# Kernel tuning notes

Hardware: AMD Instinct MI355X
Metric: run time of the kernel (lower is better)

## Reference

```python
import jax, jax.numpy as jnp
import numpy as np
import math

STRIDE = 32
CTR_CLAMP = 32.0
SCALE_CLAMP = math.log(1000.0 / 16)  # DEFAULT_SCALE_CLAMP
CONF_THRESH = 0.05
NMS_THRESH = 0.6
TOPK = 1000
NUM_CLASSES = 80
CLASS_OFFSET = 1.0e5  # separates classes so one IoU pass == per-class NMS


def setup_inputs() -> dict:
    key = jax.random.key(0)
    k1, k2 = jax.random.split(key)
    fmp_h, fmp_w = 100, 100
    A = 5
    M = fmp_h * fmp_w * A  # 50000 candidates
    cls_pred = jax.random.normal(k1, (M, NUM_CLASSES), dtype=jnp.float32)
    reg_pred = jax.random.normal(k2, (M, 4), dtype=jnp.float32)
    anchor_size = jnp.array([[32, 32], [64, 64], [128, 128], [256, 256], [512, 512]], dtype=jnp.float32)
    return {"cls_pred": cls_pred, "reg_pred": reg_pred, "anchor_size": anchor_size,
            "fmp_h": fmp_h, "fmp_w": fmp_w}


def _generate_anchors(anchor_size, fmp_h, fmp_w):
    # anchors laid out as [H*W, A, 4] -> [M, 4], matching torch.meshgrid order
    ys, xs = jnp.meshgrid(jnp.arange(fmp_h, dtype=jnp.float32),
                          jnp.arange(fmp_w, dtype=jnp.float32), indexing="ij")
    xy = (jnp.stack([xs, ys], axis=-1).reshape(-1, 2) + 0.5) * STRIDE  # [HW, 2]
    A = anchor_size.shape[0]
    anchor_xy = jnp.repeat(xy[:, None, :], A, axis=1)                   # [HW, A, 2]
    anchor_wh = jnp.broadcast_to(anchor_size[None], (xy.shape[0], A, 2))
    return jnp.concatenate([anchor_xy, anchor_wh], axis=-1).reshape(-1, 4)  # [M, 4]


def _decode_boxes(anchors, reg):
    # anchors/reg: [K, 4] (cx, cy, w, h) / (dx, dy, dw, dh)
    ctr_off = jnp.clip(reg[:, :2] * anchors[:, 2:], -CTR_CLAMP, CTR_CLAMP)
    ctr_xy = anchors[:, :2] + ctr_off
    wh = anchors[:, 2:] * jnp.exp(jnp.minimum(reg[:, 2:], SCALE_CLAMP))
    return jnp.concatenate([ctr_xy - 0.5 * wh, ctr_xy + 0.5 * wh], axis=-1)  # x1y1x2y2


def _greedy_nms_keep(boxes, valid):
    # boxes: [K, 4] already score-sorted descending; valid: [K] bool
    x1, y1, x2, y2 = boxes[:, 0], boxes[:, 1], boxes[:, 2], boxes[:, 3]
    areas = (x2 - x1) * (y2 - y1)
    xx1 = jnp.maximum(x1[:, None], x1[None, :])
    yy1 = jnp.maximum(y1[:, None], y1[None, :])
    xx2 = jnp.minimum(x2[:, None], x2[None, :])
    yy2 = jnp.minimum(y2[:, None], y2[None, :])
    inter = jnp.maximum(1e-28, xx2 - xx1) * jnp.maximum(1e-28, yy2 - yy1)
    iou = inter / (areas[:, None] + areas[None, :] - inter + 1e-14)  # [K, K]
    idxs = jnp.arange(boxes.shape[0])

    def body(i, keep):
        suppress = keep[i] & (iou[i] > NMS_THRESH) & (idxs > i)
        return keep & ~suppress

    return jax.lax.fori_loop(0, boxes.shape[0], body, valid)


def reference(cls_pred, reg_pred, anchor_size, fmp_h, fmp_w):
    anchors = _generate_anchors(anchor_size, fmp_h, fmp_w)  # [M, 4]
    probs = jax.nn.sigmoid(cls_pred)                        # [M, C]
    scores = probs.max(axis=-1)
    labels = probs.argmax(axis=-1)
    # top-k candidates (lax.top_k returns scores sorted descending)
    scores, idx = jax.lax.top_k(scores, TOPK)
    labels = labels[idx]
    reg = reg_pred[idx]
    anc = anchors[idx]
    boxes = _decode_boxes(anc, reg)                         # [K, 4] in pixels
    valid = scores >= CONF_THRESH
    # per-class NMS via class offsets (boxes of different classes never overlap)
    boxes_off = boxes + labels.astype(boxes.dtype)[:, None] * CLASS_OFFSET
    keep = _greedy_nms_keep(boxes_off, valid)
    img_w = fmp_w * STRIDE
    img_h = fmp_h * STRIDE
    scale = jnp.array([img_w, img_h, img_w, img_h], dtype=boxes.dtype)
    nboxes = jnp.clip(boxes / scale, 0.0, 1.0)
    m = keep.astype(boxes.dtype)
    return nboxes * m[:, None], scores * m, jnp.where(keep, labels, -1), keep
```

## Files before the change

kernel.cpp:

```cpp
#include <hip/hip_runtime.h>
#include <math.h>

#define NCLS 80
#define TOPK 1000
#define CAND_CAP 4096

__device__ __forceinline__ float sigmoid_np(float x) {
  float e = (float)exp(-(double)x);
  return 1.0f / (1.0f + e);
}
__device__ __forceinline__ float exp_np(float x) { return (float)exp((double)x); }

__device__ __forceinline__ unsigned fkey(float s) {
  unsigned u = __float_as_uint(s);
  return ((int)u < 0) ? ~u : (u | 0x80000000u);
}

#define KEY_BASE 0xBF000000u
__device__ __forceinline__ unsigned kbin(unsigned key) { return (key >> 11) & 0xFFFu; }

__device__ __forceinline__ void agg_add(unsigned* h, unsigned bin, bool pred) {
  unsigned long long rem = __ballot(pred);
  const int lane = threadIdx.x & 63;
  while (rem) {
    int leader = __ffsll(rem) - 1;
    unsigned lb = (unsigned)__shfl((int)bin, leader, 64);
    unsigned long long m = __ballot(pred && bin == lb);
    if (lane == leader) atomicAdd(&h[lb], (unsigned)__popcll(m));
    rem &= ~m;
  }
}

__global__ void k_zero(unsigned* __restrict__ p, int nwords) {
  int i = blockIdx.x * 256 + threadIdx.x;
  if (i < nwords) p[i] = 0u;
}

__launch_bounds__(1024)
__global__ void k_score(const float* __restrict__ cls, float* __restrict__ scores,
                        int* __restrict__ labels, unsigned* __restrict__ ghist1, int M) {
  __shared__ unsigned h1[4096];
  const int t = threadIdx.x;
  #pragma unroll
  for (int k = 0; k < 4; ++k) h1[t + 1024 * k] = 0u;
  __syncthreads();

  int gid = blockIdx.x * 1024 + t;
  int anchor = gid >> 2;
  int q = gid & 3;
  bool act = anchor < M;
  float lv[20];
  float best = -3.4e38f; int bc = 0;
  if (act) {
    const float4* row = reinterpret_cast<const float4*>(cls) + (size_t)anchor * (NCLS / 4);
    #pragma unroll
    for (int k = 0; k < 5; ++k) {
      float4 v = row[q + 4 * k];
      int cbase = (q + 4 * k) * 4;
      lv[4 * k + 0] = v.x; lv[4 * k + 1] = v.y; lv[4 * k + 2] = v.z; lv[4 * k + 3] = v.w;
      if (v.x > best) { best = v.x; bc = cbase + 0; }
      if (v.y > best) { best = v.y; bc = cbase + 1; }
      if (v.z > best) { best = v.z; bc = cbase + 2; }
      if (v.w > best) { best = v.w; bc = cbase + 3; }
    }
  } else {
    #pragma unroll
    for (int k = 0; k < 20; ++k) lv[k] = -3.4e38f;
  }
  #pragma unroll
  for (int d = 1; d < 4; d <<= 1) {
    float ob = __shfl_xor(best, d, 64);
    int oc = __shfl_xor(bc, d, 64);
    if (ob > best || (ob == best && oc < bc)) { best = ob; bc = oc; }
  }
  float s = sigmoid_np(best);
  float sp = s * (1.0f - s);
  float band = (s < 1.0f && sp > 0.0f) ? (4.8e-7f / sp) : 3.4e38f;
  float thresh = best - band;
  int cclose = 1 << 30;
  #pragma unroll
  for (int k = 0; k < 5; ++k) {
    #pragma unroll
    for (int j = 0; j < 4; ++j) {
      int c = (q + 4 * k) * 4 + j;
      if (lv[4 * k + j] >= thresh && c < cclose) cclose = c;
    }
  }
  #pragma unroll
  for (int d = 1; d < 4; d <<= 1) {
    int oc = __shfl_xor(cclose, d, 64);
    if (oc < cclose) cclose = oc;
  }
  int lab = bc;
  if (act && cclose < bc && q == 0) {
    float bp = -1.0f; int bl = 0;
    for (int c = 0; c < NCLS; ++c) {
      float p = sigmoid_np(cls[(size_t)anchor * NCLS + c]);
      if (p > bp) { bp = p; bl = c; }
    }
    lab = bl;
  }
  unsigned key = fkey(s);
  if (act && q == 0) {
    scores[anchor] = s;
    labels[anchor] = lab;
  }
  agg_add(h1, kbin(key), act && q == 0 && key >= KEY_BASE);
  __syncthreads();
  #pragma unroll
  for (int k = 0; k < 4; ++k) {
    unsigned c = h1[t + 1024 * k];
    if (c) atomicAdd(&ghist1[t + 1024 * k], c);
  }
}

__launch_bounds__(1024)
__global__ void k_compact(const unsigned* __restrict__ ghist1, const float* __restrict__ scores,
                          unsigned long long* __restrict__ cand, unsigned* __restrict__ gcount,
                          int M) {
  __shared__ unsigned chunks[1024];
  __shared__ int sB1;
  __shared__ unsigned wcnt[16];
  __shared__ unsigned sbase;
  const int t = threadIdx.x;
  const int lane = t & 63, wid = t >> 6;
  if (t == 0) sB1 = 0;

  unsigned hb0 = ghist1[4 * t], hb1 = ghist1[4 * t + 1],
           hb2 = ghist1[4 * t + 2], hb3 = ghist1[4 * t + 3];
  chunks[t] = hb0 + hb1 + hb2 + hb3;
  __syncthreads();
  for (int d = 1; d < 1024; d <<= 1) {
    unsigned v = chunks[t] + ((t + d < 1024) ? chunks[t + d] : 0u);
    __syncthreads(); chunks[t] = v; __syncthreads();
  }
  {
    unsigned ssc = chunks[t];
    unsigned ssn = (t + 1 < 1024) ? chunks[t + 1] : 0u;
    if (ssc >= (unsigned)TOPK && ssn < (unsigned)TOPK) {
      unsigned hb[4] = {hb0, hb1, hb2, hb3};
      unsigned run = ssn;
      for (int b = 3; b >= 0; --b) {
        run += hb[b];
        if (run >= (unsigned)TOPK) { sB1 = 4 * t + b; break; }
      }
    }
  }
  __syncthreads();
  const unsigned T = KEY_BASE + ((unsigned)sB1 << 11);

  int base = (blockIdx.x * 1024 + t) * 4;
  unsigned keys[4]; int idxs[4]; int np = 0;
  if (base + 3 < M) {
    float4 v = *reinterpret_cast<const float4*>(scores + base);
    unsigned kk[4] = {fkey(v.x), fkey(v.y), fkey(v.z), fkey(v.w)};
    #pragma unroll
    for (int j = 0; j < 4; ++j)
      if (kk[j] >= T) { keys[np] = kk[j]; idxs[np] = base + j; ++np; }
  } else {
    for (int i = base; i < M; ++i) {
      unsigned key = fkey(scores[i]);
      if (key >= T) { keys[np] = key; idxs[np] = i; ++np; }
    }
  }
  int sc = np;
  #pragma unroll
  for (int d = 1; d < 64; d <<= 1) {
    int o = __shfl_up(sc, d, 64);
    if (lane >= d) sc += o;
  }
  if (lane == 63) wcnt[wid] = (unsigned)sc;
  __syncthreads();
  if (t == 0) {
    unsigned acc = 0;
    for (int w = 0; w < 16; ++w) { unsigned v = wcnt[w]; wcnt[w] = acc; acc += v; }
    sbase = acc ? atomicAdd(gcount, acc) : 0u;
  }
  __syncthreads();
  unsigned pos = sbase + wcnt[wid] + (unsigned)(sc - np);
  for (int j = 0; j < np; ++j) {
    if (pos < (unsigned)CAND_CAP)
      cand[pos] = ((unsigned long long)keys[j] << 32) | (unsigned)(~(unsigned)idxs[j]);
    ++pos;
  }
}

__launch_bounds__(1024)
__global__ void k_rank(const unsigned long long* __restrict__ cand, const unsigned* __restrict__ gcount,
                       const int* __restrict__ labels, const float* __restrict__ reg,
                       const float* __restrict__ asz, const int* __restrict__ pW, int A,
                       float* __restrict__ sel_score, int* __restrict__ sel_label,
                       float* __restrict__ boxes, float* __restrict__ areas,
                       float* __restrict__ obox) {
  __shared__ unsigned long long ck[CAND_CAP];
  const int t = threadIdx.x;
  unsigned n = *gcount; if (n > (unsigned)CAND_CAP) n = (unsigned)CAND_CAP;
  for (int i = t; i < (int)n; i += 1024) ck[i] = cand[i];
  __syncthreads();
  for (int cc = 0; cc < CAND_CAP; cc += 1024) {
    if ((unsigned)cc >= n) break;
    int c = cc + t;
    bool actv = (unsigned)c < n;
    unsigned long long my = actv ? ck[c] : 0ull;
    int r = 0;
    for (int j = 0; j < (int)n; ++j) r += (ck[j] > my);
    if (actv && r < TOPK) {
      unsigned key = (unsigned)(my >> 32);
      unsigned u = (key & 0x80000000u) ? (key ^ 0x80000000u) : ~key;
      float scv = __uint_as_float(u);
      int idx = (int)(~(unsigned)my);
      int lab = labels[idx];
      int W = *pW;
      int a = idx % A;
      int cell = idx / A;
      int x = cell % W;
      int y = cell / W;
      float aw = asz[a * 2 + 0], ah = asz[a * 2 + 1];
      float ax = ((float)x + 0.5f) * 32.0f;
      float ay = ((float)y + 0.5f) * 32.0f;
      float4 rg = *reinterpret_cast<const float4*>(reg + (size_t)idx * 4);
      float offx = fminf(fmaxf(rg.x * aw, -32.0f), 32.0f);
      float offy = fminf(fmaxf(rg.y * ah, -32.0f), 32.0f);
      float cx = ax + offx, cy = ay + offy;
      const float SC = 4.135166556742356f;
      float bw = aw * exp_np(fminf(rg.z, SC));
      float bh = ah * exp_np(fminf(rg.w, SC));
      float x1 = cx - 0.5f * bw, y1 = cy - 0.5f * bh;
      float x2 = cx + 0.5f * bw, y2 = cy + 0.5f * bh;
      float off = (float)lab * 100000.0f;
      float ox1 = x1 + off, oy1 = y1 + off, ox2 = x2 + off, oy2 = y2 + off;
      sel_score[r] = scv; sel_label[r] = lab;
      boxes[r * 4 + 0] = x1; boxes[r * 4 + 1] = y1;
      boxes[r * 4 + 2] = x2; boxes[r * 4 + 3] = y2;
      obox[0 * 1024 + r] = ox1; obox[1 * 1024 + r] = oy1;
      obox[2 * 1024 + r] = ox2; obox[3 * 1024 + r] = oy2;
      areas[r] = (ox2 - ox1) * (oy2 - oy1);
    }
  }
}

__launch_bounds__(1024)
__global__ void k_mask(const float* __restrict__ obox, const float* __restrict__ areas,
                       unsigned long long* __restrict__ maskC) {
  __shared__ float so0[1024], so1[1024], so2[1024], so3[1024], sa[1024];
  const int t = threadIdx.x;
  const int c = blockIdx.x, j = t;
  so0[t] = obox[t];        so1[t] = obox[1024 + t];
  so2[t] = obox[2048 + t]; so3[t] = obox[3072 + t];
  sa[t] = areas[t];
  __syncthreads();
  unsigned long long bits = 0ull;
  if (j < TOPK) {
    float x1j = so0[j], y1j = so1[j], x2j = so2[j], y2j = so3[j];
    float aj = sa[j];
    int i0 = c * 64;
    for (int ii = 0; ii < 64; ++ii) {
      int i = i0 + ii;
      if (i < TOPK && i < j) {
        float xx1 = fmaxf(so0[i], x1j);
        float yy1 = fmaxf(so1[i], y1j);
        float xx2 = fminf(so2[i], x2j);
        float yy2 = fminf(so3[i], y2j);
        float inter = fmaxf(1e-28f, xx2 - xx1) * fmaxf(1e-28f, yy2 - yy1);
        float uni = sa[i] + aj - inter + 1e-14f;
        float iou = inter / uni;
        if (iou > 0.6f) bits |= (1ull << ii);
      }
    }
  }
  maskC[c * 1024 + j] = bits;
}

__launch_bounds__(512)
__global__ void k_nms(const unsigned long long* __restrict__ maskC,
                      const float* __restrict__ sel_score, const int* __restrict__ sel_label,
                      const float* __restrict__ boxes,
                      const int* __restrict__ pW, const int* __restrict__ pH,
                      float* __restrict__ out) {
  __shared__ unsigned long long sm[16 * 1024];
  __shared__ float ssc[1024];
  __shared__ unsigned long long kwS[16];
  const int tid = threadIdx.x;
  const int lane = tid & 63;

  {
    const float4* g4 = reinterpret_cast<const float4*>(maskC);
    float4* s4 = reinterpret_cast<float4*>(sm);
    float4 v[16];
    #pragma unroll
    for (int k = 0; k < 16; ++k) v[k] = g4[tid + k * 512];
    #pragma unroll
    for (int k = 0; k < 16; ++k) s4[tid + k * 512] = v[k];
  }
  #pragma unroll
  for (int k = 0; k < 2; ++k) {
    int i = tid + k * 512;
    ssc[i] = (i < TOPK) ? sel_score[i] : 0.0f;
  }
  __syncthreads();

  if (tid < 64) {
    unsigned long long supp[16];
    #pragma unroll
    for (int f = 0; f < 16; ++f) supp[f] = 0ull;
    #pragma unroll
    for (int f = 0; f < 16; ++f) {
      unsigned long long ct = sm[f * 1024 + f * 64 + lane];
      int r = f * 64 + lane;
      unsigned long long valid = __ballot((r < TOPK) && (ssc[r] >= 0.05f));
      unsigned long long sup_any = __ballot(ct != 0ull);
      unsigned long long avail = valid & ~supp[f];
      unsigned long long kwf = 0ull;
      while (avail) {
        unsigned long long fs = avail & sup_any;
        if (!fs) { kwf |= avail; break; }
        int i = __ffsll((long long)fs) - 1;
        unsigned long long below = (1ull << i) - 1ull;
        kwf |= avail & below;
        kwf |= (1ull << i);
        unsigned long long vict = __ballot(((ct >> i) & 1ull) != 0ull);
        avail &= ~vict;
        avail &= ~(below | (1ull << i));
      }
      if (lane == 0) kwS[f] = kwf;
      #pragma unroll
      for (int g = f + 1; g < 16; ++g)
        supp[g] |= __ballot((sm[f * 1024 + g * 64 + lane] & kwf) != 0ull);
    }
  }
  __syncthreads();

  float sw = (float)(*pW * 32);
  float sh = (float)(*pH * 32);
  const float4* b4 = reinterpret_cast<const float4*>(boxes);
  for (int r = tid; r < TOPK; r += 512) {
    bool kp = (kwS[r >> 6] >> (r & 63)) & 1ull;
    float m = kp ? 1.0f : 0.0f;
    float4 b = b4[r];
    float b0 = fminf(fmaxf(b.x / sw, 0.0f), 1.0f) * m;
    float b1 = fminf(fmaxf(b.y / sh, 0.0f), 1.0f) * m;
    float b2 = fminf(fmaxf(b.z / sw, 0.0f), 1.0f) * m;
    float b3 = fminf(fmaxf(b.w / sh, 0.0f), 1.0f) * m;
    out[r * 4 + 0] = b0; out[r * 4 + 1] = b1;
    out[r * 4 + 2] = b2; out[r * 4 + 3] = b3;
    out[TOPK * 4 + r] = ssc[r] * m;
    out[TOPK * 5 + r] = kp ? (float)sel_label[r] : -1.0f;
    out[TOPK * 6 + r] = m;
  }
}

extern "C" void kernel_launch(void* const* d_in, const int* in_sizes, int n_in,
                              void* d_out, int out_size, void* d_ws, size_t ws_size,
                              hipStream_t stream) {
  const float* cls = (const float*)d_in[0];
  const float* reg = (const float*)d_in[1];
  const float* asz = (const float*)d_in[2];
  const int* pH = (const int*)d_in[3];
  const int* pW = (const int*)d_in[4];
  int M = in_sizes[0] / NCLS;
  int A = in_sizes[2] / 2;

  char* ws = (char*)d_ws;
  size_t off = 0;
  auto alloc = [&](size_t bytes) { size_t o = off; off = (off + bytes + 255) & ~(size_t)255; return o; };
  size_t o_h1   = alloc(4096 * sizeof(unsigned));
  size_t o_cnt  = alloc(256);
  size_t zero_end = off;
  size_t o_cand = alloc((size_t)CAND_CAP * sizeof(unsigned long long));
  size_t o_sc   = alloc((size_t)M * sizeof(float));
  size_t o_lb   = alloc((size_t)M * sizeof(int));
  size_t o_ssc  = alloc(1024 * sizeof(float));
  size_t o_slb  = alloc(1024 * sizeof(int));
  size_t o_box  = alloc((size_t)TOPK * 4 * sizeof(float));
  size_t o_area = alloc(1024 * sizeof(float));
  size_t o_obox = alloc(4 * 1024 * sizeof(float));
  size_t o_mask = alloc((size_t)16 * 1024 * sizeof(unsigned long long));
  (void)ws_size; (void)out_size; (void)n_in;

  int zwords = (int)(zero_end / 4);
  k_zero<<<(zwords + 255) / 256, 256, 0, stream>>>((unsigned*)ws, zwords);
  int nblk_score = (M * 4 + 1023) / 1024;
  k_score<<<nblk_score, 1024, 0, stream>>>(
      cls, (float*)(ws + o_sc), (int*)(ws + o_lb), (unsigned*)(ws + o_h1), M);
  int nblk_cmp = ((M + 3) / 4 + 1023) / 1024;
  k_compact<<<nblk_cmp, 1024, 0, stream>>>(
      (const unsigned*)(ws + o_h1), (const float*)(ws + o_sc),
      (unsigned long long*)(ws + o_cand), (unsigned*)(ws + o_cnt), M);
  k_rank<<<1, 1024, 0, stream>>>(
      (const unsigned long long*)(ws + o_cand), (const unsigned*)(ws + o_cnt),
      (const int*)(ws + o_lb), reg, asz, pW, A,
      (float*)(ws + o_ssc), (int*)(ws + o_slb),
      (float*)(ws + o_box), (float*)(ws + o_area), (float*)(ws + o_obox));
  k_mask<<<16, 1024, 0, stream>>>(
      (const float*)(ws + o_obox), (const float*)(ws + o_area),
      (unsigned long long*)(ws + o_mask));
  k_nms<<<1, 512, 0, stream>>>(
      (const unsigned long long*)(ws + o_mask),
      (const float*)(ws + o_ssc), (const int*)(ws + o_slb),
      (const float*)(ws + o_box), pW, pH, (float*)d_out);
}
```

Before: 74.49 us.

## Fuse compact+rank and mask+NMS kernels via last-block-done pattern

Merges the candidate compaction with the ranking/decode stage, and the IoU mask stage with the greedy NMS stage. Each pair becomes one launch where the last block to finish, detected via an atomic counter and threadfence, performs the serial tail. The NMS part now loads only the upper-triangular mask tiles into a union-shared LDS buffer. This removes two kernel launches and their dependency gaps, but makes one block do the tail work while others exit, and relies on extra zeroed counters.

```diff
diff --git a/kernel.cpp b/kernel.cpp
--- a/kernel.cpp
+++ b/kernel.cpp
@@ -4,6 +4,7 @@
 #define NCLS 80
 #define TOPK 1000
 #define CAND_CAP 4096
+#define TRI_IDX(f, g) ((f) * 16 - ((f) * ((f) - 1)) / 2 + ((g) - (f)))
 
 __device__ __forceinline__ float sigmoid_np(float x) {
   float e = (float)exp(-(double)x);
@@ -115,13 +116,21 @@
 }
 
 __launch_bounds__(1024)
-__global__ void k_compact(const unsigned* __restrict__ ghist1, const float* __restrict__ scores,
-                          unsigned long long* __restrict__ cand, unsigned* __restrict__ gcount,
-                          int M) {
+__global__ void k_cr(const unsigned* __restrict__ ghist1, const float* __restrict__ scores,
+                     unsigned long long* __restrict__ cand, unsigned* __restrict__ gcount,
+                     unsigned* __restrict__ done,
+                     const int* __restrict__ labels, const float* __restrict__ reg,
+                     const float* __restrict__ asz, const int* __restrict__ pW,
+                     int M, int A,
+                     float* __restrict__ sel_score, int* __restrict__ sel_label,
+                     float* __restrict__ boxes, float* __restrict__ areas,
+                     float* __restrict__ obox) {
   __shared__ unsigned chunks[1024];
+  __shared__ unsigned long long ck[CAND_CAP];
   __shared__ int sB1;
   __shared__ unsigned wcnt[16];
   __shared__ unsigned sbase;
+  __shared__ bool sLast;
   const int t = threadIdx.x;
   const int lane = t & 63, wid = t >> 6;
   if (t == 0) sB1 = 0;
@@ -183,17 +192,14 @@
       cand[pos] = ((unsigned long long)keys[j] << 32) | (unsigned)(~(unsigned)idxs[j]);
     ++pos;
   }
-}
-
-__launch_bounds__(1024)
-__global__ void k_rank(const unsigned long long* __restrict__ cand, const unsigned* __restrict__ gcount,
-                       const int* __restrict__ labels, const float* __restrict__ reg,
-                       const float* __restrict__ asz, const int* __restrict__ pW, int A,
-                       float* __restrict__ sel_score, int* __restrict__ sel_label,
-                       float* __restrict__ boxes, float* __restrict__ areas,
-                       float* __restrict__ obox) {
-  __shared__ unsigned long long ck[CAND_CAP];
-  const int t = threadIdx.x;
+
+  __threadfence();
+  __syncthreads();
+  if (t == 0) sLast = (atomicAdd(done, 1u) == (unsigned)(gridDim.x - 1));
+  __syncthreads();
+  if (!sLast) return;
+  __threadfence();
+
   unsigned n = *gcount; if (n > (unsigned)CAND_CAP) n = (unsigned)CAND_CAP;
   for (int i = t; i < (int)n; i += 1024) ck[i] = cand[i];
   __syncthreads();
@@ -239,75 +245,82 @@
   }
 }
 
+union MnLds {
+  struct { float so0[1024], so1[1024], so2[1024], so3[1024], sa[1024]; } m;
+  struct { unsigned long long sm[8704]; float ssc[1024];
+           int pf[136], pg[136]; unsigned long long kwS[16]; } n;
+};
+
 __launch_bounds__(1024)
-__global__ void k_mask(const float* __restrict__ obox, const float* __restrict__ areas,
-                       unsigned long long* __restrict__ maskC) {
-  __shared__ float so0[1024], so1[1024], so2[1024], so3[1024], sa[1024];
+__global__ void k_mn(const float* __restrict__ obox, const float* __restrict__ areas,
+                     unsigned long long* __restrict__ maskC, unsigned* __restrict__ done,
+                     const float* __restrict__ sel_score, const int* __restrict__ sel_label,
+                     const float* __restrict__ boxes,
+                     const int* __restrict__ pW, const int* __restrict__ pH,
+                     float* __restrict__ out) {
+  __shared__ MnLds L;
+  __shared__ bool sLast;
   const int t = threadIdx.x;
+  const int lane = t & 63;
   const int c = blockIdx.x, j = t;
-  so0[t] = obox[t];        so1[t] = obox[1024 + t];
-  so2[t] = obox[2048 + t]; so3[t] = obox[3072 + t];
-  sa[t] = areas[t];
-  __syncthreads();
-  unsigned long long bits = 0ull;
-  if (j < TOPK) {
-    float x1j = so0[j], y1j = so1[j], x2j = so2[j], y2j = so3[j];
-    float aj = sa[j];
-    int i0 = c * 64;
-    for (int ii = 0; ii < 64; ++ii) {
-      int i = i0 + ii;
-      if (i < TOPK && i < j) {
-        float xx1 = fmaxf(so0[i], x1j);
-        float yy1 = fmaxf(so1[i], y1j);
-        float xx2 = fminf(so2[i], x2j);
-        float yy2 = fminf(so3[i], y2j);
-        float inter = fmaxf(1e-28f, xx2 - xx1) * fmaxf(1e-28f, yy2 - yy1);
-        float uni = sa[i] + aj - inter + 1e-14f;
-        float iou = inter / uni;
-        if (iou > 0.6f) bits |= (1ull << ii);
+
+  L.m.so0[t] = obox[t];        L.m.so1[t] = obox[1024 + t];
+  L.m.so2[t] = obox[2048 + t]; L.m.so3[t] = obox[3072 + t];
+  L.m.sa[t] = areas[t];
+  __syncthreads();
+  {
+    unsigned long long bits = 0ull;
+    if (j < TOPK) {
+      float x1j = L.m.so0[j], y1j = L.m.so1[j], x2j = L.m.so2[j], y2j = L.m.so3[j];
+      float aj = L.m.sa[j];
+      int i0 = c * 64;
+      for (int ii = 0; ii < 64; ++ii) {
+        int i = i0 + ii;
+        if (i < TOPK && i < j) {
+          float xx1 = fmaxf(L.m.so0[i], x1j);
+          float yy1 = fmaxf(L.m.so1[i], y1j);
+          float xx2 = fminf(L.m.so2[i], x2j);
+          float yy2 = fminf(L.m.so3[i], y2j);
+          float inter = fmaxf(1e-28f, xx2 - xx1) * fmaxf(1e-28f, yy2 - yy1);
+          float uni = L.m.sa[i] + aj - inter + 1e-14f;
+          float iou = inter / uni;
+          if (iou > 0.6f) bits |= (1ull << ii);
+        }
       }
     }
-  }
-  maskC[c * 1024 + j] = bits;
-}
-
-__launch_bounds__(512)
-__global__ void k_nms(const unsigned long long* __restrict__ maskC,
-                      const float* __restrict__ sel_score, const int* __restrict__ sel_label,
-                      const float* __restrict__ boxes,
-                      const int* __restrict__ pW, const int* __restrict__ pH,
-                      float* __restrict__ out) {
-  __shared__ unsigned long long sm[16 * 1024];
-  __shared__ float ssc[1024];
-  __shared__ unsigned long long kwS[16];
-  const int tid = threadIdx.x;
-  const int lane = tid & 63;
-
-  {
-    const float4* g4 = reinterpret_cast<const float4*>(maskC);
-    float4* s4 = reinterpret_cast<float4*>(sm);
-    float4 v[16];
-    #pragma unroll
-    for (int k = 0; k < 16; ++k) v[k] = g4[tid + k * 512];
-    #pragma unroll
-    for (int k = 0; k < 16; ++k) s4[tid + k * 512] = v[k];
-  }
-  #pragma unroll
-  for (int k = 0; k < 2; ++k) {
-    int i = tid + k * 512;
-    ssc[i] = (i < TOPK) ? sel_score[i] : 0.0f;
-  }
-  __syncthreads();
-
-  if (tid < 64) {
+    maskC[c * 1024 + j] = bits;
+  }
+
+  __threadfence();
+  __syncthreads();
+  if (t == 0) sLast = (atomicAdd(done, 1u) == (unsigned)(gridDim.x - 1));
+  __syncthreads();
+  if (!sLast) return;
+  __threadfence();
+  __syncthreads();
+
+  if (t < 136) {
+    int p = t, f = 0;
+    while (p >= 16 - f) { p -= 16 - f; ++f; }
+    L.n.pf[t] = f; L.n.pg[t] = f + p;
+  }
+  L.n.ssc[t] = (t < TOPK) ? sel_score[t] : 0.0f;
+  __syncthreads();
+  for (int i = t; i < 136 * 64; i += 1024) {
+    int p = i >> 6, l = i & 63;
+    L.n.sm[i] = maskC[L.n.pf[p] * 1024 + L.n.pg[p] * 64 + l];
+  }
+  __syncthreads();
+
+  if (t < 64) {
     unsigned long long supp[16];
     #pragma unroll
     for (int f = 0; f < 16; ++f) supp[f] = 0ull;
     #pragma unroll
     for (int f = 0; f < 16; ++f) {
-      unsigned long long ct = sm[f * 1024 + f * 64 + lane];
+      unsigned long long ct = L.n.sm[TRI_IDX(f, f) * 64 + lane];
       int r = f * 64 + lane;
-      unsigned long long valid = __ballot((r < TOPK) && (ssc[r] >= 0.05f));
+      unsigned long long valid = __ballot((r < TOPK) && (L.n.ssc[r] >= 0.05f));
       unsigned long long sup_any = __ballot(ct != 0ull);
       unsigned long long avail = valid & ~supp[f];
       unsigned long long kwf = 0ull;
@@ -322,10 +335,10 @@
         avail &= ~vict;
         avail &= ~(below | (1ull << i));
       }
-      if (lane == 0) kwS[f] = kwf;
+      if (lane == 0) L.n.kwS[f] = kwf;
       #pragma unroll
       for (int g = f + 1; g < 16; ++g)
-        supp[g] |= __ballot((sm[f * 1024 + g * 64 + lane] & kwf) != 0ull);
+        supp[g] |= __ballot((L.n.sm[TRI_IDX(f, g) * 64 + lane] & kwf) != 0ull);
     }
   }
   __syncthreads();
@@ -333,8 +346,9 @@
   float sw = (float)(*pW * 32);
   float sh = (float)(*pH * 32);
   const float4* b4 = reinterpret_cast<const float4*>(boxes);
-  for (int r = tid; r < TOPK; r += 512) {
-    bool kp = (kwS[r >> 6] >> (r & 63)) & 1ull;
+  if (t < TOPK) {
+    int r = t;
+    bool kp = (L.n.kwS[r >> 6] >> (r & 63)) & 1ull;
     float m = kp ? 1.0f : 0.0f;
     float4 b = b4[r];
     float b0 = fminf(fmaxf(b.x / sw, 0.0f), 1.0f) * m;
@@ -343,7 +357,7 @@
     float b3 = fminf(fmaxf(b.w / sh, 0.0f), 1.0f) * m;
     out[r * 4 + 0] = b0; out[r * 4 + 1] = b1;
     out[r * 4 + 2] = b2; out[r * 4 + 3] = b3;
-    out[TOPK * 4 + r] = ssc[r] * m;
+    out[TOPK * 4 + r] = L.n.ssc[r] * m;
     out[TOPK * 5 + r] = kp ? (float)sel_label[r] : -1.0f;
     out[TOPK * 6 + r] = m;
   }
@@ -383,19 +397,16 @@
   k_score<<<nblk_score, 1024, 0, stream>>>(
       cls, (float*)(ws + o_sc), (int*)(ws + o_lb), (unsigned*)(ws + o_h1), M);
   int nblk_cmp = ((M + 3) / 4 + 1023) / 1024;
-  k_compact<<<nblk_cmp, 1024, 0, stream>>>(
+  k_cr<<<nblk_cmp, 1024, 0, stream>>>(
       (const unsigned*)(ws + o_h1), (const float*)(ws + o_sc),
-      (unsigned long long*)(ws + o_cand), (unsigned*)(ws + o_cnt), M);
-  k_rank<<<1, 1024, 0, stream>>>(
-      (const unsigned long long*)(ws + o_cand), (const unsigned*)(ws + o_cnt),
-      (const int*)(ws + o_lb), reg, asz, pW, A,
+      (unsigned long long*)(ws + o_cand), (unsigned*)(ws + o_cnt),
+      (unsigned*)(ws + o_cnt + 4),
+      (const int*)(ws + o_lb), reg, asz, pW, M, A,
       (float*)(ws + o_ssc), (int*)(ws + o_slb),
       (float*)(ws + o_box), (float*)(ws + o_area), (float*)(ws + o_obox));
-  k_mask<<<16, 1024, 0, stream>>>(
+  k_mn<<<16, 1024, 0, stream>>>(
       (const float*)(ws + o_obox), (const float*)(ws + o_area),
-      (unsigned long long*)(ws + o_mask));
-  k_nms<<<1, 512, 0, stream>>>(
-      (const unsigned long long*)(ws + o_mask),
+      (unsigned long long*)(ws + o_mask), (unsigned*)(ws + o_cnt + 8),
       (const float*)(ws + o_ssc), (const int*)(ws + o_slb),
       (const float*)(ws + o_box), pW, pH, (float*)d_out);
 }
```

New measurement: 86.55 us. 16.2% more time.

## Fuse top-k ranking into IoU mask kernel and load only upper-triangle mask tiles

Applied to the files above, without the earlier changes.

The single-block rank kernel is merged into the 16-block mask kernel. Each block now redundantly ranks all candidates and decodes boxes into shared memory, then computes its own 64-column IoU slice, which removes one launch and the global round trip for the decoded boxes and areas. The NMS kernel grows to 1024 threads and loads only the 136 upper-triangular 64x64 mask tiles into a packed shared array instead of all 256. The cost is that the O(n^2) rank work is repeated in all 16 blocks, and the fused kernel's larger shared-memory footprint may limit occupancy.

```diff
diff --git a/kernel.cpp b/kernel.cpp
--- a/kernel.cpp
+++ b/kernel.cpp
@@ -4,6 +4,7 @@
 #define NCLS 80
 #define TOPK 1000
 #define CAND_CAP 4096
+#define TRI_IDX(f, g) ((f) * 16 - ((f) * ((f) - 1)) / 2 + ((g) - (f)))
 
 __device__ __forceinline__ float sigmoid_np(float x) {
   float e = (float)exp(-(double)x);
@@ -186,22 +187,31 @@
 }
 
 __launch_bounds__(1024)
-__global__ void k_rank(const unsigned long long* __restrict__ cand, const unsigned* __restrict__ gcount,
-                       const int* __restrict__ labels, const float* __restrict__ reg,
-                       const float* __restrict__ asz, const int* __restrict__ pW, int A,
-                       float* __restrict__ sel_score, int* __restrict__ sel_label,
-                       float* __restrict__ boxes, float* __restrict__ areas,
-                       float* __restrict__ obox) {
+__global__ void k_maskr(const unsigned long long* __restrict__ cand,
+                        const unsigned* __restrict__ gcount,
+                        const int* __restrict__ labels, const float* __restrict__ reg,
+                        const float* __restrict__ asz, const int* __restrict__ pW, int A,
+                        float* __restrict__ sel_score, int* __restrict__ sel_label,
+                        float* __restrict__ boxes,
+                        unsigned long long* __restrict__ maskC) {
   __shared__ unsigned long long ck[CAND_CAP];
+  __shared__ float so0[1024], so1[1024], so2[1024], so3[1024], sa[1024];
+  __shared__ float4 bx[1024];
+  __shared__ float ssc[1024]; __shared__ int slab[1024];
   const int t = threadIdx.x;
+  const int c = blockIdx.x;
+
+  ssc[t] = 0.0f; slab[t] = 0;
+  so0[t] = 0.0f; so1[t] = 0.0f; so2[t] = 0.0f; so3[t] = 0.0f; sa[t] = 0.0f;
   unsigned n = *gcount; if (n > (unsigned)CAND_CAP) n = (unsigned)CAND_CAP;
   for (int i = t; i < (int)n; i += 1024) ck[i] = cand[i];
   __syncthreads();
+
   for (int cc = 0; cc < CAND_CAP; cc += 1024) {
     if ((unsigned)cc >= n) break;
-    int c = cc + t;
-    bool actv = (unsigned)c < n;
-    unsigned long long my = actv ? ck[c] : 0ull;
+    int cidx = cc + t;
+    bool actv = (unsigned)cidx < n;
+    unsigned long long my = actv ? ck[cidx] : 0ull;
     int r = 0;
     for (int j = 0; j < (int)n; ++j) r += (ck[j] > my);
     if (actv && r < TOPK) {
@@ -229,83 +239,78 @@
       float x2 = cx + 0.5f * bw, y2 = cy + 0.5f * bh;
       float off = (float)lab * 100000.0f;
       float ox1 = x1 + off, oy1 = y1 + off, ox2 = x2 + off, oy2 = y2 + off;
-      sel_score[r] = scv; sel_label[r] = lab;
-      boxes[r * 4 + 0] = x1; boxes[r * 4 + 1] = y1;
-      boxes[r * 4 + 2] = x2; boxes[r * 4 + 3] = y2;
-      obox[0 * 1024 + r] = ox1; obox[1 * 1024 + r] = oy1;
-      obox[2 * 1024 + r] = ox2; obox[3 * 1024 + r] = oy2;
-      areas[r] = (ox2 - ox1) * (oy2 - oy1);
-    }
+      ssc[r] = scv; slab[r] = lab;
+      bx[r] = make_float4(x1, y1, x2, y2);
+      so0[r] = ox1; so1[r] = oy1; so2[r] = ox2; so3[r] = oy2;
+      sa[r] = (ox2 - ox1) * (oy2 - oy1);
+    }
+  }
+  __syncthreads();
+
+  if (c == 0) {
+    sel_score[t] = ssc[t];
+    sel_label[t] = slab[t];
+    reinterpret_cast<float4*>(boxes)[t] = bx[t];
+  }
+
+  {
+    int j = t;
+    unsigned long long bits = 0ull;
+    if (j < TOPK) {
+      float x1j = so0[j], y1j = so1[j], x2j = so2[j], y2j = so3[j];
+      float aj = sa[j];
+      int i0 = c * 64;
+      for (int ii = 0; ii < 64; ++ii) {
+        int i = i0 + ii;
+        if (i < TOPK && i < j) {
+          float xx1 = fmaxf(so0[i], x1j);
+          float yy1 = fmaxf(so1[i], y1j);
+          float xx2 = fminf(so2[i], x2j);
+          float yy2 = fminf(so3[i], y2j);
+          float inter = fmaxf(1e-28f, xx2 - xx1) * fmaxf(1e-28f, yy2 - yy1);
+          float uni = sa[i] + aj - inter + 1e-14f;
+          float iou = inter / uni;
+          if (iou > 0.6f) bits |= (1ull << ii);
+        }
+      }
+    }
+    maskC[c * 1024 + j] = bits;
   }
 }
 
 __launch_bounds__(1024)
-__global__ void k_mask(const float* __restrict__ obox, const float* __restrict__ areas,
-                       unsigned long long* __restrict__ maskC) {
-  __shared__ float so0[1024], so1[1024], so2[1024], so3[1024], sa[1024];
-  const int t = threadIdx.x;
-  const int c = blockIdx.x, j = t;
-  so0[t] = obox[t];        so1[t] = obox[1024 + t];
-  so2[t] = obox[2048 + t]; so3[t] = obox[3072 + t];
-  sa[t] = areas[t];
-  __syncthreads();
-  unsigned long long bits = 0ull;
-  if (j < TOPK) {
-    float x1j = so0[j], y1j = so1[j], x2j = so2[j], y2j = so3[j];
-    float aj = sa[j];
-    int i0 = c * 64;
-    for (int ii = 0; ii < 64; ++ii) {
-      int i = i0 + ii;
-      if (i < TOPK && i < j) {
-        float xx1 = fmaxf(so0[i], x1j);
-        float yy1 = fmaxf(so1[i], y1j);
-        float xx2 = fminf(so2[i], x2j);
-        float yy2 = fminf(so3[i], y2j);
-        float inter = fmaxf(1e-28f, xx2 - xx1) * fmaxf(1e-28f, yy2 - yy1);
-        float uni = sa[i] + aj - inter + 1e-14f;
-        float iou = inter / uni;
-        if (iou > 0.6f) bits |= (1ull << ii);
-      }
-    }
-  }
-  maskC[c * 1024 + j] = bits;
-}
-
-__launch_bounds__(512)
 __global__ void k_nms(const unsigned long long* __restrict__ maskC,
                       const float* __restrict__ sel_score, const int* __restrict__ sel_label,
                       const float* __restrict__ boxes,
                       const int* __restrict__ pW, const int* __restrict__ pH,
                       float* __restrict__ out) {
-  __shared__ unsigned long long sm[16 * 1024];
+  __shared__ unsigned long long sm[136 * 64];
   __shared__ float ssc[1024];
   __shared__ unsigned long long kwS[16];
-  const int tid = threadIdx.x;
-  const int lane = tid & 63;
-
-  {
-    const float4* g4 = reinterpret_cast<const float4*>(maskC);
-    float4* s4 = reinterpret_cast<float4*>(sm);
-    float4 v[16];
-    #pragma unroll
-    for (int k = 0; k < 16; ++k) v[k] = g4[tid + k * 512];
-    #pragma unroll
-    for (int k = 0; k < 16; ++k) s4[tid + k * 512] = v[k];
-  }
-  #pragma unroll
-  for (int k = 0; k < 2; ++k) {
-    int i = tid + k * 512;
-    ssc[i] = (i < TOPK) ? sel_score[i] : 0.0f;
-  }
-  __syncthreads();
-
-  if (tid < 64) {
+  __shared__ int pf[136], pg[136];
+  const int t = threadIdx.x;
+  const int lane = t & 63;
+
+  if (t < 136) {
+    int p = t, f = 0;
+    while (p >= 16 - f) { p -= 16 - f; ++f; }
+    pf[t] = f; pg[t] = f + p;
+  }
+  ssc[t] = (t < TOPK) ? sel_score[t] : 0.0f;
+  __syncthreads();
+  for (int i = t; i < 136 * 64; i += 1024) {
+    int p = i >> 6, l = i & 63;
+    sm[i] = maskC[pf[p] * 1024 + pg[p] * 64 + l];
+  }
+  __syncthreads();
+
+  if (t < 64) {
     unsigned long long supp[16];
     #pragma unroll
     for (int f = 0; f < 16; ++f) supp[f] = 0ull;
     #pragma unroll
     for (int f = 0; f < 16; ++f) {
-      unsigned long long ct = sm[f * 1024 + f * 64 + lane];
+      unsigned long long ct = sm[TRI_IDX(f, f) * 64 + lane];
       int r = f * 64 + lane;
       unsigned long long valid = __ballot((r < TOPK) && (ssc[r] >= 0.05f));
       unsigned long long sup_any = __ballot(ct != 0ull);
@@ -325,7 +330,7 @@
       if (lane == 0) kwS[f] = kwf;
       #pragma unroll
       for (int g = f + 1; g < 16; ++g)
-        supp[g] |= __ballot((sm[f * 1024 + g * 64 + lane] & kwf) != 0ull);
+        supp[g] |= __ballot((sm[TRI_IDX(f, g) * 64 + lane] & kwf) != 0ull);
     }
   }
   __syncthreads();
@@ -333,7 +338,8 @@
   float sw = (float)(*pW * 32);
   float sh = (float)(*pH * 32);
   const float4* b4 = reinterpret_cast<const float4*>(boxes);
-  for (int r = tid; r < TOPK; r += 512) {
+  if (t < TOPK) {
+    int r = t;
     bool kp = (kwS[r >> 6] >> (r & 63)) & 1ull;
     float m = kp ? 1.0f : 0.0f;
     float4 b = b4[r];
@@ -371,9 +377,7 @@
   size_t o_lb   = alloc((size_t)M * sizeof(int));
   size_t o_ssc  = alloc(1024 * sizeof(float));
   size_t o_slb  = alloc(1024 * sizeof(int));
-  size_t o_box  = alloc((size_t)TOPK * 4 * sizeof(float));
-  size_t o_area = alloc(1024 * sizeof(float));
-  size_t o_obox = alloc(4 * 1024 * sizeof(float));
+  size_t o_box  = alloc(1024 * 4 * sizeof(float));
   size_t o_mask = alloc((size_t)16 * 1024 * sizeof(unsigned long long));
   (void)ws_size; (void)out_size; (void)n_in;
 
@@ -386,15 +390,12 @@
   k_compact<<<nblk_cmp, 1024, 0, stream>>>(
       (const unsigned*)(ws + o_h1), (const float*)(ws + o_sc),
       (unsigned long long*)(ws + o_cand), (unsigned*)(ws + o_cnt), M);
-  k_rank<<<1, 1024, 0, stream>>>(
+  k_maskr<<<16, 1024, 0, stream>>>(
       (const unsigned long long*)(ws + o_cand), (const unsigned*)(ws + o_cnt),
       (const int*)(ws + o_lb), reg, asz, pW, A,
-      (float*)(ws + o_ssc), (int*)(ws + o_slb),
-      (float*)(ws + o_box), (float*)(ws + o_area), (float*)(ws + o_obox));
-  k_mask<<<16, 1024, 0, stream>>>(
-      (const float*)(ws + o_obox), (const float*)(ws + o_area),
+      (float*)(ws + o_ssc), (int*)(ws + o_slb), (float*)(ws + o_box),
       (unsigned long long*)(ws + o_mask));
-  k_nms<<<1, 512, 0, stream>>>(
+  k_nms<<<1, 1024, 0, stream>>>(
       (const unsigned long long*)(ws + o_mask),
       (const float*)(ws + o_ssc), (const int*)(ws + o_slb),
       (const float*)(ws + o_box), pW, pH, (float*)d_out);
```

Result: no change. 73.16 us (-1.8%).
